# Kernel tuning notes

Measured on AMD Instinct MI355X. Metric: run time of the kernel, lower is better.

Reference implementation:

```python
import jax, jax.numpy as jnp
import numpy as np

H = 4      # num_heads (== num_v_heads)
DK = 128   # head_k_dim
DV = 256   # head_v_dim = head_dim * expand_v
NH = 2     # num_householder
HID = 1024 # hidden_size
KSZ = 4    # conv_size
EPS = 1e-5 # norm_eps


def short_conv(x, w):
    """Causal depthwise conv1d + SiLU. x: [B,T,C], w: [C,K]."""
    K = w.shape[1]
    T = x.shape[1]
    xp = jnp.pad(x, ((0, 0), (K - 1, 0), (0, 0)))
    y = sum(xp[:, i:i + T, :] * w[:, i] for i in range(K))
    return jax.nn.silu(y)


def l2norm(x, eps=1e-6):
    return x * jax.lax.rsqrt(jnp.sum(x * x, axis=-1, keepdims=True) + eps)


def setup_inputs() -> dict:
    key = jax.random.key(0)
    ks = jax.random.split(key, 16)
    s = 0.02
    B, T = 2, 1024
    return {
        "hidden_states": jax.random.normal(ks[0], (B, T, HID), jnp.float32),
        "Wq": jax.random.normal(ks[1], (HID, H * DK), jnp.float32) * s,
        "Wk": jax.random.normal(ks[2], (HID, NH * H * DK), jnp.float32) * s,
        "Wv": jax.random.normal(ks[3], (HID, NH * H * DV), jnp.float32) * s,
        "Wb": jax.random.normal(ks[4], (HID, NH * H), jnp.float32) * s,
        "Wa": jax.random.normal(ks[5], (HID, H), jnp.float32) * s,
        "Wg": jax.random.normal(ks[6], (HID, H * DV), jnp.float32) * s,
        "Wo": jax.random.normal(ks[7], (H * DV, HID), jnp.float32) * s,
        "A_log": jnp.log(jax.random.uniform(ks[8], (H,), jnp.float32, 0.5, 8.0)),
        "dt_bias": jax.random.normal(ks[9], (H,), jnp.float32) * 0.1,
        "wq_conv": jax.random.normal(ks[10], (H * DK, KSZ), jnp.float32) * 0.2,
        "wk_conv": jax.random.normal(ks[11], (NH * H * DK, KSZ), jnp.float32) * 0.2,
        "wv_conv": jax.random.normal(ks[12], (NH * H * DV, KSZ), jnp.float32) * 0.2,
        "o_norm_weight": jnp.ones((DV,), jnp.float32),
    }


def reference(hidden_states, Wq, Wk, Wv, Wb, Wa, Wg, Wo, A_log, dt_bias,
              wq_conv, wk_conv, wv_conv, o_norm_weight):
    B, T, _ = hidden_states.shape
    # projections + short conv (+ SiLU)
    q = short_conv(hidden_states @ Wq, wq_conv).reshape(B, T, H, DK)
    k = short_conv(hidden_states @ Wk, wk_conv).reshape(B, T, NH, H, DK)
    v = short_conv(hidden_states @ Wv, wv_conv).reshape(B, T, NH, H, DV)
    q = l2norm(q)
    k = l2norm(k)
    # beta: sigmoid * 2 (allow_neg_eigval), layout '(n h)'
    beta = 2.0 * jax.nn.sigmoid(hidden_states @ Wb).reshape(B, T, NH, H)
    # forget gate per token/head
    g = -jnp.exp(A_log) * jax.nn.softplus(hidden_states @ Wa + dt_bias)  # [B,T,H]

    def step(S, x):
        # S: [B,H,DK,DV]
        q_t, k_t, v_t, b_t, g_t = x
        S = S * jnp.exp(g_t)[..., None, None]  # token-level decay
        for i in range(NH):  # sequential Householder delta updates
            ki, vi, bi = k_t[:, i], v_t[:, i], b_t[:, i]
            kv = jnp.einsum('bhk,bhkv->bhv', ki, S)
            S = S + bi[..., None, None] * jnp.einsum('bhk,bhv->bhkv', ki, vi - kv)
        o_t = jnp.einsum('bhk,bhkv->bhv', q_t, S)
        return S, o_t

    xs = (q.transpose(1, 0, 2, 3), k.transpose(1, 0, 2, 3, 4),
          v.transpose(1, 0, 2, 3, 4), beta.transpose(1, 0, 2, 3),
          g.transpose(1, 0, 2))
    S0 = jnp.zeros((B, H, DK, DV), hidden_states.dtype)
    _, o = jax.lax.scan(jax.checkpoint(step), S0, xs)
    o = o.transpose(1, 0, 2, 3)  # [B,T,H,DV]

    # gated RMSNorm (FusedRMSNormGated): rmsnorm(o)*w * silu(gate)
    gate = (hidden_states @ Wg).reshape(B, T, H, DV)
    o = o * jax.lax.rsqrt(jnp.mean(o * o, axis=-1, keepdims=True) + EPS) * o_norm_weight
    o = o * jax.nn.silu(gate)
    return o.reshape(B, T, H * DV) @ Wo
```

## Files before the change

### kernel.cpp

```cpp
#include <hip/hip_runtime.h>
#include <cstdint>
#include <cstddef>

#define H 4
#define DK 128
#define DV 256
#define NH 2
#define HID 1024
#define KSZ 4
#define NTOT 4608

typedef __bf16 bfx8 __attribute__((ext_vector_type(8)));
typedef float f32x4 __attribute__((ext_vector_type(4)));

typedef __attribute__((address_space(1))) const void GVOID;
typedef __attribute__((address_space(3))) void LVOID;
#define GLL(g, l) __builtin_amdgcn_global_load_lds((GVOID*)(g), (LVOID*)(l), 16, 0, 0)

__device__ __forceinline__ float wave_sum(float x) {
#pragma unroll
  for (int off = 1; off < 64; off <<= 1) x += __shfl_xor(x, off, 64);
  return x;
}

__device__ __forceinline__ ushort f2bf(float x) {
  uint u = __float_as_uint(x);
  return (ushort)((u + 0x7fffu + ((u >> 16) & 1u)) >> 16);
}

#define DPP_ADD(x, ctrl) \
  x += __int_as_float(__builtin_amdgcn_update_dpp(0, __float_as_int(x), ctrl, 0xf, 0xf, true))

template <int N>
__device__ __forceinline__ void dpp_reduce(float (&d)[N]) {
#pragma unroll
  for (int i = 0; i < N; i++) DPP_ADD(d[i], 0x111);
#pragma unroll
  for (int i = 0; i < N; i++) DPP_ADD(d[i], 0x112);
#pragma unroll
  for (int i = 0; i < N; i++) DPP_ADD(d[i], 0x114);
#pragma unroll
  for (int i = 0; i < N; i++) DPP_ADD(d[i], 0x118);
#pragma unroll
  for (int i = 0; i < N; i++) DPP_ADD(d[i], 0x142);
#pragma unroll
  for (int i = 0; i < N; i++) DPP_ADD(d[i], 0x143);
#pragma unroll
  for (int i = 0; i < N; i++)
    d[i] = __int_as_float(__builtin_amdgcn_readlane(__float_as_int(d[i]), 63));
}

__global__ __launch_bounds__(256) void cast_hs(const float* __restrict__ src,
                                               ushort* __restrict__ dst) {
  int i = blockIdx.x * 256 + threadIdx.x;
  float4 v = ((const float4*)src)[i];
  ushort4 o = {f2bf(v.x), f2bf(v.y), f2bf(v.z), f2bf(v.w)};
  ((ushort4*)dst)[i] = o;
}

__global__ __launch_bounds__(256) void tr_pack(const float* __restrict__ Wq,
                                               const float* __restrict__ Wk,
                                               const float* __restrict__ Wv,
                                               const float* __restrict__ Wg,
                                               ushort* __restrict__ Bt) {
  __shared__ float tile[32][33];
  int n0 = blockIdx.x * 32, k0 = blockIdx.y * 32;
  const float* src;
  int ld, nb;
  if (n0 < 512)       { src = Wq; ld = 512;  nb = n0; }
  else if (n0 < 1536) { src = Wk; ld = 1024; nb = n0 - 512; }
  else if (n0 < 3584) { src = Wv; ld = 2048; nb = n0 - 1536; }
  else                { src = Wg; ld = 1024; nb = n0 - 3584; }
  int tx = threadIdx.x & 31, ty = threadIdx.x >> 5;
#pragma unroll
  for (int i = 0; i < 4; i++)
    tile[ty + i * 8][tx] = src[(size_t)(k0 + ty + i * 8) * ld + nb + tx];
  __syncthreads();
#pragma unroll
  for (int i = 0; i < 4; i++)
    Bt[(size_t)(n0 + ty + i * 8) * 1024 + k0 + tx] = f2bf(tile[tx][ty + i * 8]);
}

__global__ __launch_bounds__(256) void tr_one(const float* __restrict__ W,
                                              ushort* __restrict__ Bt, int N) {
  __shared__ float tile[32][33];
  int n0 = blockIdx.x * 32, k0 = blockIdx.y * 32;
  int tx = threadIdx.x & 31, ty = threadIdx.x >> 5;
#pragma unroll
  for (int i = 0; i < 4; i++)
    tile[ty + i * 8][tx] = W[(size_t)(k0 + ty + i * 8) * N + n0 + tx];
  __syncthreads();
#pragma unroll
  for (int i = 0; i < 4; i++)
    Bt[(size_t)(n0 + ty + i * 8) * 1024 + k0 + tx] = f2bf(tile[tx][ty + i * 8]);
}

__global__ __launch_bounds__(256) void gemm_bf16(const ushort* __restrict__ A,
                                                 const ushort* __restrict__ Bt,
                                                 float* __restrict__ C,
                                                 int K, int ldc) {
  __shared__ __align__(16) ushort As[128][32];
  __shared__ __align__(16) ushort Bs[128][32];
  const int tid = threadIdx.x;
  const int lane = tid & 63, wave = tid >> 6;
  const int wr = wave >> 1, wc = wave & 1;
  const int row0 = blockIdx.y * 128, col0 = blockIdx.x * 128;

  const int ra = wave * 32 + (lane >> 2);
  const int rb = ra + 16;
  const int kc = (lane & 3) * 8;
  const ushort* pa0 = A + (size_t)(row0 + ra) * K + kc;
  const ushort* pa1 = A + (size_t)(row0 + rb) * K + kc;
  const ushort* pb0 = Bt + (size_t)(col0 + ra) * K + kc;
  const ushort* pb1 = Bt + (size_t)(col0 + rb) * K + kc;
  ushort* lA0 = &As[wave * 32][0];
  ushort* lA1 = &As[wave * 32 + 16][0];
  ushort* lB0 = &Bs[wave * 32][0];
  ushort* lB1 = &Bs[wave * 32 + 16][0];

  f32x4 acc[4][4];
#pragma unroll
  for (int i = 0; i < 4; i++)
#pragma unroll
    for (int j = 0; j < 4; j++) acc[i][j] = {0.f, 0.f, 0.f, 0.f};

  const int lrow = lane & 15, lk = (lane >> 4) * 8;

  for (int k0 = 0; k0 < K; k0 += 32) {
    __syncthreads();
    GLL(pa0, lA0);
    GLL(pa1, lA1);
    GLL(pb0, lB0);
    GLL(pb1, lB1);
    pa0 += 32; pa1 += 32; pb0 += 32; pb1 += 32;
    __syncthreads();
    bfx8 af[4], bf[4];
#pragma unroll
    for (int mf = 0; mf < 4; mf++)
      af[mf] = *(const bfx8*)&As[wr * 64 + mf * 16 + lrow][lk];
#pragma unroll
    for (int nf = 0; nf < 4; nf++)
      bf[nf] = *(const bfx8*)&Bs[wc * 64 + nf * 16 + lrow][lk];
#pragma unroll
    for (int mf = 0; mf < 4; mf++)
#pragma unroll
      for (int nf = 0; nf < 4; nf++)
        acc[mf][nf] = __builtin_amdgcn_mfma_f32_16x16x32_bf16(af[mf], bf[nf], acc[mf][nf], 0, 0, 0);
  }
  const int crow = (lane >> 4) * 4, ccol = lane & 15;
#pragma unroll
  for (int mf = 0; mf < 4; mf++)
#pragma unroll
    for (int nf = 0; nf < 4; nf++)
#pragma unroll
      for (int rr = 0; rr < 4; rr++)
        C[(size_t)(row0 + wr * 64 + mf * 16 + crow + rr) * ldc + col0 + wc * 64 + nf * 16 + ccol] =
            acc[mf][nf][rr];
}

__global__ __launch_bounds__(256) void proj_bg(const float* __restrict__ hs,
                                               const float* __restrict__ Wb,
                                               const float* __restrict__ Wa,
                                               const float* __restrict__ A_log,
                                               const float* __restrict__ dt_bias,
                                               float* __restrict__ beta,
                                               float* __restrict__ g) {
  int row = blockIdx.x;
  int lane = threadIdx.x & 63;
  int wave = threadIdx.x >> 6;
  const float* x = hs + (size_t)row * HID;
  for (int out = wave; out < 12; out += 4) {
    float sum = 0.f;
    if (out < 8) {
      for (int k = lane; k < HID; k += 64) sum = fmaf(x[k], Wb[(size_t)k * 8 + out], sum);
    } else {
      int c = out - 8;
      for (int k = lane; k < HID; k += 64) sum = fmaf(x[k], Wa[(size_t)k * 4 + c], sum);
    }
    sum = wave_sum(sum);
    if (lane == 0) {
      if (out < 8) {
        beta[(size_t)row * 8 + out] = 2.f / (1.f + expf(-sum));
      } else {
        int h = out - 8;
        float xx = sum + dt_bias[h];
        float sp = (xx > 20.f) ? xx : log1pf(expf(xx));
        g[(size_t)row * 4 + h] = expf(-expf(A_log[h]) * sp);
      }
    }
  }
}

__global__ __launch_bounds__(128) void conv_q(const float* __restrict__ x, int ldx,
                                              const float* __restrict__ w,
                                              float* __restrict__ y, int T) {
  int rb = blockIdx.x;
  int h = rb % 4;
  int bt = rb / 4;
  int t = bt % T;
  int b = bt / T;
  int d = threadIdx.x;
  int c = h * 128 + d;
  const float* wc = w + (size_t)c * KSZ;
  float acc = 0.f;
#pragma unroll
  for (int i = 0; i < KSZ; i++) {
    int tt = t - (KSZ - 1) + i;
    if (tt >= 0) acc = fmaf(x[(size_t)(b * T + tt) * ldx + c], wc[i], acc);
  }
  float val = acc / (1.f + expf(-acc));
  float ss = wave_sum(val * val);
  __shared__ float sred[2];
  if ((threadIdx.x & 63) == 0) sred[threadIdx.x >> 6] = ss;
  __syncthreads();
  val *= rsqrtf(sred[0] + sred[1] + 1e-6f);
  y[((size_t)(b * 512 + (t >> 1)) * 4 + h) * 256 + (d >> 1) * 4 + (d & 1) + (t & 1) * 2] = val;
}

__global__ __launch_bounds__(128) void conv_k(const float* __restrict__ x, int ldx,
                                              const float* __restrict__ w,
                                              float* __restrict__ y, int T) {
  int rb = blockIdx.x;
  int gi = rb % 8;
  int bt = rb / 8;
  int t = bt % T;
  int b = bt / T;
  int i = gi >> 2, h = gi & 3;
  int d = threadIdx.x;
  int c = i * 512 + h * 128 + d;
  const float* wc = w + (size_t)c * KSZ;
  float acc = 0.f;
#pragma unroll
  for (int kk = 0; kk < KSZ; kk++) {
    int tt = t - (KSZ - 1) + kk;
    if (tt >= 0) acc = fmaf(x[(size_t)(b * T + tt) * ldx + c], wc[kk], acc);
  }
  float val = acc / (1.f + expf(-acc));
  float ss = wave_sum(val * val);
  __shared__ float sred[2];
  if ((threadIdx.x & 63) == 0) sred[threadIdx.x >> 6] = ss;
  __syncthreads();
  val *= rsqrtf(sred[0] + sred[1] + 1e-6f);
  y[((size_t)(b * T + t) * 4 + h) * 256 + (d >> 1) * 4 + (d & 1) + i * 2] = val;
}

__global__ __launch_bounds__(256) void conv_v(const float* __restrict__ x, int ldx,
                                              const float* __restrict__ w,
                                              float* __restrict__ y, int T) {
  int rb = blockIdx.x;
  int gi = rb % 8;
  int bt = rb / 8;
  int t = bt % T;
  int b = bt / T;
  int i = gi >> 2, h = gi & 3;
  int d = threadIdx.x;
  int c = i * 1024 + h * 256 + d;
  const float* wc = w + (size_t)c * KSZ;
  float acc = 0.f;
#pragma unroll
  for (int kk = 0; kk < KSZ; kk++) {
    int tt = t - (KSZ - 1) + kk;
    if (tt >= 0) acc = fmaf(x[(size_t)(b * T + tt) * ldx + c], wc[kk], acc);
  }
  float val = acc / (1.f + expf(-acc));
  y[((size_t)(b * 512 + (t >> 1)) * 4 + h) * 1024 + d * 4 + (t & 1) * 2 + i] = val;
}

__global__ __launch_bounds__(256) void cross_dots2(const float* __restrict__ kbuf2,
                                                   const float* __restrict__ qbuf2,
                                                   const float* __restrict__ beta,
                                                   const float* __restrict__ gam,
                                                   float* __restrict__ rec) {
  int idx = blockIdx.x * 4 + (threadIdx.x >> 6);
  int lane = threadIdx.x & 63;
  int h = idx & 3, tp = (idx >> 2) & 511, b = idx >> 11;
  int t = 2 * tp;
  const float4 kA = *(const float4*)&kbuf2[((size_t)(b * 1024 + t) * 4 + h) * 256 + lane * 4];
  const float4 kB = *(const float4*)&kbuf2[((size_t)(b * 1024 + t + 1) * 4 + h) * 256 + lane * 4];
  const float4 qv = *(const float4*)&qbuf2[(size_t)idx * 256 + lane * 4];
  float d[12];
  d[0] = kA.z * kA.x + kA.w * kA.y;
  d[1] = kB.x * kA.x + kB.y * kA.y;
  d[2] = kB.x * kA.z + kB.y * kA.w;
  d[3] = kB.z * kA.x + kB.w * kA.y;
  d[4] = kB.z * kA.z + kB.w * kA.w;
  d[5] = kB.z * kB.x + kB.w * kB.y;
  d[6] = qv.x * kA.x + qv.y * kA.y;
  d[7] = qv.x * kA.z + qv.y * kA.w;
  d[8] = qv.z * kA.x + qv.w * kA.y;
  d[9] = qv.z * kA.z + qv.w * kA.w;
  d[10] = qv.z * kB.x + qv.w * kB.y;
  d[11] = qv.z * kB.z + qv.w * kB.w;
  dpp_reduce(d);
  int bt = b * 1024 + t;
  float b0 = beta[(size_t)(bt * 2 + 0) * 4 + h];
  float b1 = beta[(size_t)(bt * 2 + 1) * 4 + h];
  float b2 = beta[(size_t)(bt * 2 + 2) * 4 + h];
  float b3 = beta[(size_t)(bt * 2 + 3) * 4 + h];
  float gt = gam[(size_t)bt * 4 + h];
  float gt1 = gam[(size_t)(bt + 1) * 4 + h];
  if (lane == 0) {
    float G2 = gt * gt1;
    float4* rp = (float4*)&rec[(size_t)idx * 24];
    rp[0] = {b0 * gt, b1 * gt, b1 * d[0], gt};
    rp[1] = {b2 * G2, b2 * gt1 * d[1], b2 * gt1 * d[2], gt1};
    rp[2] = {b3 * G2, b3 * gt1 * d[3], b3 * gt1 * d[4], b3 * d[5]};
    rp[3] = {d[6], d[7], G2, b0};
    rp[4] = {gt1 * d[8], gt1 * d[9], d[10], d[11]};
    rp[5] = {b1, b2, b3, 0.f};
  }
}

__global__ __launch_bounds__(256, 2) void scan2(const float4* __restrict__ kb,
                                                const float4* __restrict__ qb,
                                                const float4* __restrict__ vb,
                                                const float4* __restrict__ rb,
                                                float* __restrict__ o) {
  const int lane = threadIdx.x & 63;
  const int wave = __builtin_amdgcn_readfirstlane(threadIdx.x >> 6);
  const int bh = blockIdx.x & 7;
  const int cb = blockIdx.x >> 3;
  const int b = bh >> 2, h = bh & 3;
  const int col = cb * 4 + wave;

  const float4* kp = kb + ((size_t)(b * 1024) * 4 + h) * 64 + lane + 128;
  const float4* qp = qb + ((size_t)(b * 512) * 4 + h) * 64 + lane;
  const float4* vp = vb + ((size_t)(b * 512) * 4 + h) * 256 + col;
  const float4* rp = rb + ((size_t)(b * 512) * 4 + h) * 6;
  float* op = o + (size_t)(b * 1024) * NTOT + h * 256 + col;

  float sx = 0.f, sy = 0.f;

  float4 AkA, AkB, Aqv, Avv, AR0, AR1, AR2, AR3, AR4, AR5;
  float4 BkA, BkB, Bqv, Bvv, BR0, BR1, BR2, BR3, BR4, BR5;

#define LOADQ(P) { \
    P##kA = kp[-128]; \
    P##kB = kp[128]; \
    P##qv = qp[0]; \
    P##vv = vp[0]; \
    P##R0 = rp[0]; \
    P##R1 = rp[1]; \
    P##R2 = rp[2]; \
    P##R3 = rp[3]; \
    P##R4 = rp[4]; \
    P##R5 = rp[5]; \
    kp += 512; qp += 256; vp += 1024; rp += 24; \
    __builtin_amdgcn_sched_barrier(0); }

#define STEPQ(P) { \
    float r[6]; \
    r[0] = P##kA.x * sx + P##kA.y * sy; \
    r[1] = P##kA.z * sx + P##kA.w * sy; \
    r[2] = P##kB.x * sx + P##kB.y * sy; \
    r[3] = P##kB.z * sx + P##kB.w * sy; \
    r[4] = P##qv.x * sx + P##qv.y * sy; \
    r[5] = P##qv.z * sx + P##qv.w * sy; \
    dpp_reduce(r); \
    float c0 = fmaf(-P##R0.x, r[0], P##R3.w * P##vv.x); \
    float c1 = fmaf(-P##R0.z, c0, fmaf(-P##R0.y, r[1], P##R5.x * P##vv.y)); \
    float c2 = fmaf(-P##R1.z, c1, fmaf(-P##R1.y, c0, fmaf(-P##R1.x, r[2], P##R5.y * P##vv.z))); \
    float c3 = fmaf(-P##R2.w, c2, fmaf(-P##R2.z, c1, fmaf(-P##R2.y, c0, \
               fmaf(-P##R2.x, r[3], P##R5.z * P##vv.w)))); \
    float ot = fmaf(P##R3.y, c1, fmaf(P##R3.x, c0, P##R0.w * r[4])); \
    float ot1 = fmaf(P##R4.w, c3, fmaf(P##R4.z, c2, fmaf(P##R4.y, c1, \
                fmaf(P##R4.x, c0, P##R3.z * r[5])))); \
    float g0 = P##R1.w * c0, g1 = P##R1.w * c1; \
    sx = fmaf(c3, P##kB.z, fmaf(c2, P##kB.x, fmaf(g1, P##kA.z, fmaf(g0, P##kA.x, P##R3.z * sx)))); \
    sy = fmaf(c3, P##kB.w, fmaf(c2, P##kB.y, fmaf(g1, P##kA.w, fmaf(g0, P##kA.y, P##R3.z * sy)))); \
    if (lane == 0) { op[0] = ot; op[NTOT] = ot1; } \
    op += 2 * NTOT; }

  LOADQ(A)
  LOADQ(B)
  for (int it = 0; it < 255; ++it) {
    STEPQ(A) LOADQ(A)
    STEPQ(B) LOADQ(B)
  }
  STEPQ(A)
  STEPQ(B)
#undef LOADQ
#undef STEPQ
}

__global__ __launch_bounds__(256) void post_norm_gate(const float* __restrict__ o,
                                                      const float* __restrict__ gate,
                                                      const float* __restrict__ w,
                                                      ushort* __restrict__ obf) {
  int rb = blockIdx.x;
  int bt = rb >> 2, h = rb & 3;
  int tid = threadIdx.x;
  size_t ob = (size_t)bt * NTOT + h * 256 + tid;
  float ov = o[ob];
  float ss = wave_sum(ov * ov);
  __shared__ float sred[4];
  if ((tid & 63) == 0) sred[tid >> 6] = ss;
  __syncthreads();
  float tot = sred[0] + sred[1] + sred[2] + sred[3];
  float rms = rsqrtf(tot * (1.f / 256.f) + 1e-5f);
  float gt = gate[(size_t)bt * NTOT + h * 256 + tid];
  float val = ov * rms * w[tid] * (gt / (1.f + expf(-gt)));
  obf[(size_t)bt * HID + h * 256 + tid] = f2bf(val);
}

extern "C" void kernel_launch(void* const* d_in, const int* in_sizes, int n_in,
                              void* d_out, int out_size, void* d_ws, size_t ws_size,
                              hipStream_t stream) {
  const float* hs      = (const float*)d_in[0];
  const float* Wq      = (const float*)d_in[1];
  const float* Wk      = (const float*)d_in[2];
  const float* Wv      = (const float*)d_in[3];
  const float* Wb      = (const float*)d_in[4];
  const float* Wa      = (const float*)d_in[5];
  const float* Wg      = (const float*)d_in[6];
  const float* Wo      = (const float*)d_in[7];
  const float* A_log   = (const float*)d_in[8];
  const float* dt_bias = (const float*)d_in[9];
  const float* wq_conv = (const float*)d_in[10];
  const float* wk_conv = (const float*)d_in[11];
  const float* wv_conv = (const float*)d_in[12];
  const float* o_w     = (const float*)d_in[13];
  float* out = (float*)d_out;

  const int B = 2, T = 1024, M = B * T;

  float* ws    = (float*)d_ws;
  float* qkvg  = ws;
  float* kbuf  = qkvg + (size_t)M * NTOT;
  float* vbuf  = kbuf + (size_t)M * 1024;
  float* betab = vbuf + (size_t)M * 2048;
  float* gb    = betab + (size_t)M * 8;
  float* recb  = gb + (size_t)M * 4;
  float* qbuf  = out;

  ushort* bqkvgT = (ushort*)kbuf;
  ushort* hsb    = (ushort*)(vbuf + (size_t)524288);
  ushort* woT = (ushort*)kbuf;
  ushort* obf = (ushort*)vbuf;

  cast_hs<<<(M * HID / 4) / 256, 256, 0, stream>>>(hs, hsb);
  tr_pack<<<dim3(NTOT / 32, HID / 32), 256, 0, stream>>>(Wq, Wk, Wv, Wg, bqkvgT);
  gemm_bf16<<<dim3(NTOT / 128, M / 128), 256, 0, stream>>>(hsb, bqkvgT, qkvg, HID, NTOT);
  proj_bg<<<M, 256, 0, stream>>>(hs, Wb, Wa, A_log, dt_bias, betab, gb);
  conv_q<<<M * 4, 128, 0, stream>>>(qkvg + 0, NTOT, wq_conv, qbuf, T);
  conv_k<<<M * 8, 128, 0, stream>>>(qkvg + 512, NTOT, wk_conv, kbuf, T);
  conv_v<<<M * 8, 256, 0, stream>>>(qkvg + 1536, NTOT, wv_conv, vbuf, T);
  cross_dots2<<<M * H / 8, 256, 0, stream>>>(kbuf, qbuf, betab, gb, recb);
  scan2<<<512, 256, 0, stream>>>((const float4*)kbuf, (const float4*)qbuf,
                                 (const float4*)vbuf, (const float4*)recb, qkvg);
  post_norm_gate<<<M * H, 256, 0, stream>>>(qkvg, qkvg + 3584, o_w, obf);
  tr_one<<<dim3(HID / 32, HID / 32), 256, 0, stream>>>(Wo, woT, HID);
  gemm_bf16<<<dim3(HID / 128, M / 128), 256, 0, stream>>>(obf, woT, out, HID, HID);
}
```

Before: 419.6 us.

## Fuse q/k/v short-conv kernels into one kernel with sliding time window

```diff
diff --git a/kernel.cpp b/kernel.cpp
--- a/kernel.cpp
+++ b/kernel.cpp
@@ -191,79 +191,61 @@
   }
 }
 
-__global__ __launch_bounds__(128) void conv_q(const float* __restrict__ x, int ldx,
-                                              const float* __restrict__ w,
-                                              float* __restrict__ y, int T) {
-  int rb = blockIdx.x;
-  int h = rb % 4;
-  int bt = rb / 4;
-  int t = bt % T;
-  int b = bt / T;
-  int d = threadIdx.x;
-  int c = h * 128 + d;
-  const float* wc = w + (size_t)c * KSZ;
-  float acc = 0.f;
-#pragma unroll
-  for (int i = 0; i < KSZ; i++) {
-    int tt = t - (KSZ - 1) + i;
-    if (tt >= 0) acc = fmaf(x[(size_t)(b * T + tt) * ldx + c], wc[i], acc);
+__global__ __launch_bounds__(256) void conv_all(const float* __restrict__ x,
+                                                const float* __restrict__ wqc,
+                                                const float* __restrict__ wkc,
+                                                const float* __restrict__ wvc,
+                                                float* __restrict__ yq,
+                                                float* __restrict__ yk,
+                                                float* __restrict__ yv, int T) {
+  int blk = blockIdx.x;
+  int cg = blk % 14;
+  int tc = (blk / 14) % 64;
+  int b  = blk / (14 * 64);
+  int tid = threadIdx.x;
+  int c = cg * 256 + tid;
+  int t0 = tc * 16;
+  const int lane = tid & 63, wav = tid >> 6;
+
+  int region, h, d, ii = 0;
+  const float* wp;
+  if (c < 512)       { region = 0; h = c >> 7; d = c & 127; wp = wqc + (size_t)c * 4; }
+  else if (c < 1536) { int ck = c - 512;  region = 1; ii = ck >> 9;  h = (ck >> 7) & 3; d = ck & 127; wp = wkc + (size_t)ck * 4; }
+  else               { int cv = c - 1536; region = 2; ii = cv >> 10; h = (cv >> 8) & 3; d = cv & 255; wp = wvc + (size_t)cv * 4; }
+  float4 wcv = *(const float4*)wp;
+
+  const float* xp = x + (size_t)(b * T) * NTOT + c;
+#define XLD(t) (((t) >= 0) ? xp[(size_t)(t) * NTOT] : 0.f)
+  float w0 = XLD(t0 - 3), w1 = XLD(t0 - 2), w2 = XLD(t0 - 1);
+
+  __shared__ float sred[4];
+
+  for (int tt = 0; tt < 16; ++tt) {
+    int t = t0 + tt;
+    float w3 = XLD(t);
+    float acc = 0.f;
+    acc = fmaf(w0, wcv.x, acc);
+    acc = fmaf(w1, wcv.y, acc);
+    acc = fmaf(w2, wcv.z, acc);
+    acc = fmaf(w3, wcv.w, acc);
+    float val = acc / (1.f + expf(-acc));
+    if (region != 2) {
+      float ss = wave_sum(val * val);
+      if (lane == 0) sred[wav] = ss;
+      __syncthreads();
+      float tot = sred[(tid >> 7) * 2] + sred[(tid >> 7) * 2 + 1];
+      __syncthreads();
+      val *= rsqrtf(tot + 1e-6f);
+    }
+    if (region == 0)
+      yq[((size_t)(b * 512 + (t >> 1)) * 4 + h) * 256 + (d >> 1) * 4 + (d & 1) + (t & 1) * 2] = val;
+    else if (region == 1)
+      yk[((size_t)(b * T + t) * 4 + h) * 256 + (d >> 1) * 4 + (d & 1) + ii * 2] = val;
+    else
+      yv[((size_t)(b * 512 + (t >> 1)) * 4 + h) * 1024 + d * 4 + (t & 1) * 2 + ii] = val;
+    w0 = w1; w1 = w2; w2 = w3;
   }
-  float val = acc / (1.f + expf(-acc));
-  float ss = wave_sum(val * val);
-  __shared__ float sred[2];
-  if ((threadIdx.x & 63) == 0) sred[threadIdx.x >> 6] = ss;
-  __syncthreads();
-  val *= rsqrtf(sred[0] + sred[1] + 1e-6f);
-  y[((size_t)(b * 512 + (t >> 1)) * 4 + h) * 256 + (d >> 1) * 4 + (d & 1) + (t & 1) * 2] = val;
-}
-
-__global__ __launch_bounds__(128) void conv_k(const float* __restrict__ x, int ldx,
-                                              const float* __restrict__ w,
-                                              float* __restrict__ y, int T) {
-  int rb = blockIdx.x;
-  int gi = rb % 8;
-  int bt = rb / 8;
-  int t = bt % T;
-  int b = bt / T;
-  int i = gi >> 2, h = gi & 3;
-  int d = threadIdx.x;
-  int c = i * 512 + h * 128 + d;
-  const float* wc = w + (size_t)c * KSZ;
-  float acc = 0.f;
-#pragma unroll
-  for (int kk = 0; kk < KSZ; kk++) {
-    int tt = t - (KSZ - 1) + kk;
-    if (tt >= 0) acc = fmaf(x[(size_t)(b * T + tt) * ldx + c], wc[kk], acc);
-  }
-  float val = acc / (1.f + expf(-acc));
-  float ss = wave_sum(val * val);
-  __shared__ float sred[2];
-  if ((threadIdx.x & 63) == 0) sred[threadIdx.x >> 6] = ss;
-  __syncthreads();
-  val *= rsqrtf(sred[0] + sred[1] + 1e-6f);
-  y[((size_t)(b * T + t) * 4 + h) * 256 + (d >> 1) * 4 + (d & 1) + i * 2] = val;
-}
-
-__global__ __launch_bounds__(256) void conv_v(const float* __restrict__ x, int ldx,
-                                              const float* __restrict__ w,
-                                              float* __restrict__ y, int T) {
-  int rb = blockIdx.x;
-  int gi = rb % 8;
-  int bt = rb / 8;
-  int t = bt % T;
-  int b = bt / T;
-  int i = gi >> 2, h = gi & 3;
-  int d = threadIdx.x;
-  int c = i * 1024 + h * 256 + d;
-  const float* wc = w + (size_t)c * KSZ;
-  float acc = 0.f;
-#pragma unroll
-  for (int kk = 0; kk < KSZ; kk++) {
-    int tt = t - (KSZ - 1) + kk;
-    if (tt >= 0) acc = fmaf(x[(size_t)(b * T + tt) * ldx + c], wc[kk], acc);
-  }
-  float val = acc / (1.f + expf(-acc));
-  y[((size_t)(b * 512 + (t >> 1)) * 4 + h) * 1024 + d * 4 + (t & 1) * 2 + i] = val;
+#undef XLD
 }
 
 __global__ __launch_bounds__(256) void cross_dots2(const float* __restrict__ kbuf2,
@@ -442,9 +424,8 @@
   tr_pack<<<dim3(NTOT / 32, HID / 32), 256, 0, stream>>>(Wq, Wk, Wv, Wg, bqkvgT);
   gemm_bf16<<<dim3(NTOT / 128, M / 128), 256, 0, stream>>>(hsb, bqkvgT, qkvg, HID, NTOT);
   proj_bg<<<M, 256, 0, stream>>>(hs, Wb, Wa, A_log, dt_bias, betab, gb);
-  conv_q<<<M * 4, 128, 0, stream>>>(qkvg + 0, NTOT, wq_conv, qbuf, T);
-  conv_k<<<M * 8, 128, 0, stream>>>(qkvg + 512, NTOT, wk_conv, kbuf, T);
-  conv_v<<<M * 8, 256, 0, stream>>>(qkvg + 1536, NTOT, wv_conv, vbuf, T);
+  conv_all<<<2 * 64 * 14, 256, 0, stream>>>(qkvg, wq_conv, wk_conv, wv_conv,
+                                            qbuf, kbuf, vbuf, T);
   cross_dots2<<<M * H / 8, 256, 0, stream>>>(kbuf, qbuf, betab, gb, recb);
   scan2<<<512, 256, 0, stream>>>((const float4*)kbuf, (const float4*)qbuf,
                                  (const float4*)vbuf, (const float4*)recb, qkvg);
```

New measurement: 394.7 us. 1.06x faster.
